# Kernel optimization log

Hardware: AMD Instinct MI355X
Metric: run time of the kernel (lower is better)

The kernel has to match this reference:

```python
import jax, jax.numpy as jnp
import numpy as np

THRESH = 1.0      # membrane_threshold
DECAY = 0.95      # membrane_decay
REFRAC = 2.0      # refractory_period
LR = 0.001        # learning_rate
MAX_RATE = 100.0  # max_spike_rate
DT = 1.0          # time_step (ms)


def _lif(v, r, I):
    """Event-driven LIF update, vectorized over (batch, neuron).
    Neurons are only updated where input current > 0 (as in the original
    gated per-element loop); elsewhere state is frozen.
    """
    active = I > 0
    refrac = r > 0
    v_int = v * DECAY + I
    fired = active & (~refrac) & (v_int >= THRESH)
    v_new = jnp.where(~active, v, jnp.where(refrac | fired, 0.0, v_int))
    r_new = jnp.where(~active, r,
                      jnp.where(refrac, r - 1.0,
                                jnp.where(fired, REFRAC, r)))
    return v_new, r_new, fired.astype(I.dtype)


def setup_inputs() -> dict:
    key = jax.random.key(0)
    k1, k2, k3, k4 = jax.random.split(key, 4)
    B, In, H, Out, T = 128, 1024, 4096, 1024, 100
    x = jax.random.uniform(k1, (B, In), dtype=jnp.float32)
    W1 = jax.random.normal(k2, (H, In), dtype=jnp.float32) / np.float32(np.sqrt(In))
    W2 = jax.random.normal(k3, (Out, H), dtype=jnp.float32) / np.float32(np.sqrt(H))
    noise = jax.random.uniform(k4, (T, B, In), dtype=jnp.float32)
    return {"x": x, "W1": W1, "W2": W2, "noise": noise, "time_steps": T}


def reference(x, W1, W2, noise, time_steps):
    B, In = x.shape
    H = W1.shape[0]
    Out = W2.shape[0]
    # rate coding: Bernoulli spikes per time step  -> (T, B, In)
    probs = jnp.clip(x * MAX_RATE, 0.0, MAX_RATE) * (DT / 1000.0)
    spikes_in = (noise < probs[None]).astype(x.dtype)

    def step(carry, inp):
        v_i, r_i, v_h, r_h, v_o, r_o, W1c, tp, tn, acc = carry
        t, s_in = inp
        # input layer LIF (current = encoded spikes)
        v_i, r_i, in_spk = _lif(v_i, r_i, s_in)
        # hidden layer: current = input spikes @ W1^T
        hid_I = in_spk @ W1c.T                      # (B, H)
        v_h, r_h, hid_spk = _lif(v_h, r_h, hid_I)
        # output layer: current = hidden spikes @ W2^T
        out_I = hid_spk @ W2.T                      # (B, Out)
        v_o, r_o, out_spk = _lif(v_o, r_o, out_I)
        acc = acc + out_spk
        # STDP every 10 steps
        stdp = (t % 10) == 0
        pre_m = in_spk.mean(0)                      # (In,)
        post_m = hid_spk.mean(0)                    # (H,)
        tp_n = 0.9 * tp + pre_m
        tn_n = 0.9 * tn + post_m
        tp = jnp.where(stdp, tp_n, tp)
        tn = jnp.where(stdp, tn_n, tn)
        both = (in_spk.sum() > 0) & (hid_spk.sum() > 0)
        dW = LR * (jnp.outer(tp_n, post_m).T - jnp.outer(pre_m, tn_n).T)  # (H, In)
        W1_new = jnp.clip(W1c + dW, -1.0, 1.0)
        W1c = jnp.where(stdp & both, W1_new, W1c)
        return (v_i, r_i, v_h, r_h, v_o, r_o, W1c, tp, tn, acc), None

    z = lambda *s: jnp.zeros(s, x.dtype)
    carry0 = (z(B, In), z(B, In), z(B, H), z(B, H), z(B, Out), z(B, Out),
              W1, z(In), z(H), z(B, Out))
    xs = (jnp.arange(time_steps), spikes_in)
    carry, _ = jax.lax.scan(step, carry0, xs)
    out_counts = carry[-1]
    return out_counts / time_steps
```

## Files before the change

### kernel.cpp

```cpp
#include <hip/hip_runtime.h>
#include <cstdint>
#include <cstddef>

#define BB   128
#define IN   1024
#define HID  4096
#define OUTN 1024
#define TSTEPS 100
#define KC   384

__global__ __launch_bounds__(256) void ttrans_k(const float* __restrict__ src,
                                                float* __restrict__ dst,
                                                int R, int C) {
  __shared__ float tile[32][33];
  int tx = threadIdx.x & 31;
  int ty = threadIdx.x >> 5;
  int c0 = blockIdx.x * 32, r0 = blockIdx.y * 32;
  #pragma unroll
  for (int j = 0; j < 32; j += 8)
    tile[ty + j][tx] = src[(size_t)(r0 + ty + j) * C + (c0 + tx)];
  __syncthreads();
  #pragma unroll
  for (int j = 0; j < 32; j += 8)
    dst[(size_t)(c0 + ty + j) * R + (r0 + tx)] = tile[tx][ty + j];
}

__device__ __forceinline__ unsigned char lif_f32(float I, float& v, float& r) {
  bool active = I > 0.0f;
  bool refrac = r > 0.0f;
  float vi = __fadd_rn(__fmul_rn(v, 0.95f), I);
  bool fired = active && !refrac && (vi >= 1.0f);
  float vn = !active ? v : ((refrac || fired) ? 0.0f : vi);
  float rn = !active ? r : (refrac ? (r - 1.0f) : (fired ? 2.0f : r));
  v = vn; r = rn;
  return fired ? (unsigned char)1 : (unsigned char)0;
}

__device__ __forceinline__ void hidden_body(
    int bx, int b, int tid,
    const float* __restrict__ noise_t, const float* __restrict__ x,
    const float* __restrict__ rin_in, float* __restrict__ rin_out,
    unsigned char* __restrict__ in_spk,
    const float* __restrict__ W1T,
    float* __restrict__ v_h, float* __restrict__ r_h,
    unsigned char* __restrict__ hid_spk,
    unsigned short* s_idx, int* s_off, int* wsum) {
  size_t ebase = (size_t)b * IN + (size_t)tid * 4;
  const float4 xv = *reinterpret_cast<const float4*>(x + ebase);
  const float4 nv = *reinterpret_cast<const float4*>(noise_t + ebase);
  const float4 rv = *reinterpret_cast<const float4*>(rin_in + ebase);
  float px[4] = {xv.x, xv.y, xv.z, xv.w};
  float pn[4] = {nv.x, nv.y, nv.z, nv.w};
  float pr[4] = {rv.x, rv.y, rv.z, rv.w};
  int f[4]; float rn[4];
  #pragma unroll
  for (int j = 0; j < 4; j++) {
    float p = __fmul_rn(px[j], 100.0f);
    p = fminf(fmaxf(p, 0.0f), 100.0f);
    p = __fmul_rn(p, 0.001f);
    bool s = pn[j] < p;
    bool refrac = pr[j] > 0.0f;
    bool fired = s && !refrac;
    rn[j] = !s ? pr[j] : (refrac ? (pr[j] - 1.0f) : 2.0f);
    f[j] = fired ? 1 : 0;
  }
  if (bx == 0) {
    *reinterpret_cast<float4*>(rin_out + ebase) = make_float4(rn[0], rn[1], rn[2], rn[3]);
    uchar4 sp; sp.x = (unsigned char)f[0]; sp.y = (unsigned char)f[1];
    sp.z = (unsigned char)f[2]; sp.w = (unsigned char)f[3];
    *reinterpret_cast<uchar4*>(in_spk + ebase) = sp;
  }
  int cnt = f[0] + f[1] + f[2] + f[3];

  int lane = tid & 63, wv = tid >> 6;
  int inc = cnt;
  #pragma unroll
  for (int d = 1; d < 64; d <<= 1) {
    int nn = __shfl_up(inc, d, 64);
    if (lane >= d) inc += nn;
  }
  if (lane == 63) wsum[wv] = inc;
  __syncthreads();
  int wbase = 0;
  #pragma unroll
  for (int w = 0; w < 4; w++) if (w < wv) wbase += wsum[w];
  int excl = wbase + inc - cnt;

  int o = excl, kb = tid * 4;
  if (f[0]) s_idx[o++] = (unsigned short)(kb);
  if (f[1]) s_idx[o++] = (unsigned short)(kb + 1);
  if (f[2]) s_idx[o++] = (unsigned short)(kb + 2);
  if (f[3]) s_idx[o++] = (unsigned short)(kb + 3);
  if (tid == 0)   s_off[0] = 0;
  if (tid == 96)  s_off[1] = excl;
  if (tid == 192) s_off[2] = excl;
  if (tid == 255) s_off[3] = excl + cnt;
  __syncthreads();

  int h0 = bx * 1024 + tid * 4;
  const char* Wb = (const char*)W1T;
  unsigned cb = (unsigned)h0 << 2;
  float t0 = 0.0f, t1 = 0.0f, t2 = 0.0f, t3 = 0.0f;
  #pragma unroll
  for (int p = 0; p < 3; p++) {
    int ks = s_off[p], ke = s_off[p + 1];
    float a0 = 0.0f, a1 = 0.0f, a2 = 0.0f, a3 = 0.0f;
    int k = ks;
    for (; k + 4 <= ke; k += 4) {
      unsigned o0 = ((unsigned)s_idx[k]     << 14) + cb;
      unsigned o1 = ((unsigned)s_idx[k + 1] << 14) + cb;
      unsigned o2 = ((unsigned)s_idx[k + 2] << 14) + cb;
      unsigned o3 = ((unsigned)s_idx[k + 3] << 14) + cb;
      float4 w0 = *reinterpret_cast<const float4*>(Wb + o0);
      float4 w1 = *reinterpret_cast<const float4*>(Wb + o1);
      float4 w2 = *reinterpret_cast<const float4*>(Wb + o2);
      float4 w3 = *reinterpret_cast<const float4*>(Wb + o3);
      a0 = __fadd_rn(a0, w0.x); a1 = __fadd_rn(a1, w0.y);
      a2 = __fadd_rn(a2, w0.z); a3 = __fadd_rn(a3, w0.w);
      a0 = __fadd_rn(a0, w1.x); a1 = __fadd_rn(a1, w1.y);
      a2 = __fadd_rn(a2, w1.z); a3 = __fadd_rn(a3, w1.w);
      a0 = __fadd_rn(a0, w2.x); a1 = __fadd_rn(a1, w2.y);
      a2 = __fadd_rn(a2, w2.z); a3 = __fadd_rn(a3, w2.w);
      a0 = __fadd_rn(a0, w3.x); a1 = __fadd_rn(a1, w3.y);
      a2 = __fadd_rn(a2, w3.z); a3 = __fadd_rn(a3, w3.w);
    }
    for (; k < ke; k++) {
      unsigned oo = ((unsigned)s_idx[k] << 14) + cb;
      float4 w = *reinterpret_cast<const float4*>(Wb + oo);
      a0 = __fadd_rn(a0, w.x); a1 = __fadd_rn(a1, w.y);
      a2 = __fadd_rn(a2, w.z); a3 = __fadd_rn(a3, w.w);
    }
    t0 = __fadd_rn(t0, a0); t1 = __fadd_rn(t1, a1);
    t2 = __fadd_rn(t2, a2); t3 = __fadd_rn(t3, a3);
  }
  size_t idx = (size_t)b * HID + h0;
  float4 vv = *reinterpret_cast<float4*>(v_h + idx);
  float4 rr = *reinterpret_cast<float4*>(r_h + idx);
  uchar4 sp;
  sp.x = lif_f32(t0, vv.x, rr.x);
  sp.y = lif_f32(t1, vv.y, rr.y);
  sp.z = lif_f32(t2, vv.z, rr.z);
  sp.w = lif_f32(t3, vv.w, rr.w);
  *reinterpret_cast<float4*>(v_h + idx) = vv;
  *reinterpret_cast<float4*>(r_h + idx) = rr;
  *reinterpret_cast<uchar4*>(hid_spk + idx) = sp;
}

__device__ __forceinline__ void out_body(
    int bx, int b, int tid,
    const unsigned char* __restrict__ hid_spk,
    const float* __restrict__ W2T,
    float* __restrict__ v_o, float* __restrict__ r_o,
    float* __restrict__ out_acc,
    unsigned short* s_idx, int* s_off, int* wsum, float* parts) {
  int lane = tid & 63, kg = tid >> 6;

  uint4 u = *reinterpret_cast<const uint4*>(hid_spk + (size_t)b * HID + tid * 16);
  unsigned ww[4] = {u.x, u.y, u.z, u.w};
  int cnt = 0;
  #pragma unroll
  for (int j = 0; j < 16; j++) cnt += (ww[j >> 2] >> ((j & 3) * 8)) & 0xff;

  int inc = cnt;
  #pragma unroll
  for (int d = 1; d < 64; d <<= 1) {
    int nn = __shfl_up(inc, d, 64);
    if (lane >= d) inc += nn;
  }
  if (lane == 63) wsum[kg] = inc;
  __syncthreads();
  int wbase = 0;
  #pragma unroll
  for (int w = 0; w < 4; w++) if (w < kg) wbase += wsum[w];
  int excl = wbase + inc - cnt;

  int oo = excl, kb = tid * 16;
  #pragma unroll
  for (int j = 0; j < 16; j++) {
    if ((ww[j >> 2] >> ((j & 3) * 8)) & 0xff) s_idx[oo++] = (unsigned short)(kb + j);
  }
  if ((tid % 24) == 0 && tid <= 240) s_off[tid / 24] = excl;
  if (tid == 255) s_off[11] = excl + cnt;
  __syncthreads();

  const int pstart = (kg == 0) ? 0 : (kg == 1) ? 3 : (kg == 2) ? 6 : 9;
  const int pend   = (kg == 0) ? 3 : (kg == 1) ? 6 : (kg == 2) ? 9 : 11;
  int col0 = lane * 4;
  const char* Wb = (const char*)W2T;
  unsigned cb = ((unsigned)(bx * 256 + col0)) << 2;
  for (int p = pstart; p < pend; p++) {
    int ks = s_off[p], ke = s_off[p + 1];
    float a0 = 0.0f, a1 = 0.0f, a2 = 0.0f, a3 = 0.0f;
    int k = ks;
    for (; k + 4 <= ke; k += 4) {
      unsigned o0 = ((unsigned)s_idx[k]     << 12) + cb;
      unsigned o1 = ((unsigned)s_idx[k + 1] << 12) + cb;
      unsigned o2 = ((unsigned)s_idx[k + 2] << 12) + cb;
      unsigned o3 = ((unsigned)s_idx[k + 3] << 12) + cb;
      float4 w0 = *reinterpret_cast<const float4*>(Wb + o0);
      float4 w1 = *reinterpret_cast<const float4*>(Wb + o1);
      float4 w2 = *reinterpret_cast<const float4*>(Wb + o2);
      float4 w3 = *reinterpret_cast<const float4*>(Wb + o3);
      a0 = __fadd_rn(a0, w0.x); a1 = __fadd_rn(a1, w0.y);
      a2 = __fadd_rn(a2, w0.z); a3 = __fadd_rn(a3, w0.w);
      a0 = __fadd_rn(a0, w1.x); a1 = __fadd_rn(a1, w1.y);
      a2 = __fadd_rn(a2, w1.z); a3 = __fadd_rn(a3, w1.w);
      a0 = __fadd_rn(a0, w2.x); a1 = __fadd_rn(a1, w2.y);
      a2 = __fadd_rn(a2, w2.z); a3 = __fadd_rn(a3, w2.w);
      a0 = __fadd_rn(a0, w3.x); a1 = __fadd_rn(a1, w3.y);
      a2 = __fadd_rn(a2, w3.z); a3 = __fadd_rn(a3, w3.w);
    }
    for (; k < ke; k++) {
      unsigned ob = ((unsigned)s_idx[k] << 12) + cb;
      float4 w = *reinterpret_cast<const float4*>(Wb + ob);
      a0 = __fadd_rn(a0, w.x); a1 = __fadd_rn(a1, w.y);
      a2 = __fadd_rn(a2, w.z); a3 = __fadd_rn(a3, w.w);
    }
    *reinterpret_cast<float4*>(parts + p * 256 + col0) = make_float4(a0, a1, a2, a3);
  }
  __syncthreads();

  float total = 0.0f;
  #pragma unroll
  for (int p = 0; p < 11; p++) total = __fadd_rn(total, parts[p * 256 + tid]);
  int o = bx * 256 + tid;
  size_t idx = (size_t)b * OUTN + o;
  float v = v_o[idx], r = r_o[idx];
  unsigned char fired = lif_f32(total, v, r);
  v_o[idx] = v; r_o[idx] = r;
  if (fired) out_acc[idx] = __fadd_rn(out_acc[idx], 1.0f);
}

__global__ __launch_bounds__(256) void hidden_k(
    const float* __restrict__ noise_t, const float* __restrict__ x,
    const float* __restrict__ rin_in, float* __restrict__ rin_out,
    unsigned char* __restrict__ in_spk,
    const float* __restrict__ W1T,
    float* __restrict__ v_h, float* __restrict__ r_h,
    unsigned char* __restrict__ hid_spk) {
  __shared__ unsigned short s_idx[IN];
  __shared__ int s_off[4];
  __shared__ int wsum[4];
  hidden_body(blockIdx.x, blockIdx.y, threadIdx.x, noise_t, x, rin_in, rin_out,
              in_spk, W1T, v_h, r_h, hid_spk, s_idx, s_off, wsum);
}

__global__ __launch_bounds__(256) void out_k(
    const unsigned char* __restrict__ hid_spk, const float* __restrict__ W2T,
    float* __restrict__ v_o, float* __restrict__ r_o, float* __restrict__ out_acc) {
  __shared__ unsigned short s_idx[HID];
  __shared__ int s_off[12];
  __shared__ int wsum[4];
  __shared__ float parts[11 * 256];
  out_body(blockIdx.x, blockIdx.y, threadIdx.x, hid_spk, W2T, v_o, r_o, out_acc,
           s_idx, s_off, wsum, parts);
}

__global__ __launch_bounds__(256) void step_k(
    const float* __restrict__ noise_t, const float* __restrict__ x,
    const float* __restrict__ rin_in, float* __restrict__ rin_out,
    unsigned char* __restrict__ in_spk,
    const float* __restrict__ W1T,
    float* __restrict__ v_h, float* __restrict__ r_h,
    unsigned char* __restrict__ hid_spk_w,
    const unsigned char* __restrict__ hid_spk_r,
    const float* __restrict__ W2T,
    float* __restrict__ v_o, float* __restrict__ r_o, float* __restrict__ out_acc) {
  __shared__ __align__(16) unsigned char smem[19520];
  int b = blockIdx.y;
  if (blockIdx.x < 4) {
    unsigned short* s_idx = (unsigned short*)smem;
    int* s_off = (int*)(smem + 2048);
    int* wsum  = (int*)(smem + 2064);
    hidden_body(blockIdx.x, b, threadIdx.x, noise_t, x, rin_in, rin_out,
                in_spk, W1T, v_h, r_h, hid_spk_w, s_idx, s_off, wsum);
  } else {
    unsigned short* s_idx = (unsigned short*)smem;
    int* s_off = (int*)(smem + 8192);
    int* wsum  = (int*)(smem + 8240);
    float* parts = (float*)(smem + 8256);
    out_body(blockIdx.x - 4, b, threadIdx.x, hid_spk_r, W2T, v_o, r_o, out_acc,
             s_idx, s_off, wsum, parts);
  }
}

#define NWSTAT ((IN + HID) / 4)
__global__ __launch_bounds__(256) void stats1_k(
    const unsigned char* __restrict__ in_spk, const unsigned char* __restrict__ hid_spk,
    unsigned* __restrict__ pcnt) {
  int w = blockIdx.x * 256 + threadIdx.x;
  int r0 = blockIdx.y * 16;
  unsigned s = 0;
  if (w < IN / 4) {
    const unsigned* p = (const unsigned*)in_spk;
    #pragma unroll
    for (int b = 0; b < 16; b++) s += p[(size_t)(r0 + b) * (IN / 4) + w];
  } else {
    const unsigned* p = (const unsigned*)hid_spk;
    int w2 = w - IN / 4;
    #pragma unroll
    for (int b = 0; b < 16; b++) s += p[(size_t)(r0 + b) * (HID / 4) + w2];
  }
  atomicAdd(pcnt + w, s);
}

__global__ __launch_bounds__(256) void stats2_k(
    const unsigned* __restrict__ pcnt,
    float* __restrict__ pre_m, float* __restrict__ post_m,
    float* __restrict__ tp, float* __restrict__ tn, int* __restrict__ flags) {
  int c = blockIdx.x * 256 + threadIdx.x;
  int cnt = (int)((pcnt[c >> 2] >> ((c & 3) * 8)) & 0xff);
  int lane = threadIdx.x & 63;
  if (c < IN) {
    float pm = __fdiv_rn((float)cnt, 128.0f);
    pre_m[c] = pm;
    tp[c] = __fadd_rn(__fmul_rn(0.9f, tp[c]), pm);
    unsigned long long any = __ballot(cnt > 0);
    if (any && lane == 0) atomicOr(flags + 0, 1);
  } else {
    int h = c - IN;
    float pm = __fdiv_rn((float)cnt, 128.0f);
    post_m[h] = pm;
    tn[h] = __fadd_rn(__fmul_rn(0.9f, tn[h]), pm);
    unsigned long long any = __ballot(cnt > 0);
    if (any && lane == 0) atomicOr(flags + 1, 1);
  }
}

__global__ __launch_bounds__(256) void apply_k(
    float* __restrict__ W1T,
    const float* __restrict__ tp, const float* __restrict__ tn,
    const float* __restrict__ pre_m, const float* __restrict__ post_m,
    const int* __restrict__ flags) {
  if (!(flags[0] && flags[1])) return;
  size_t idx = (size_t)blockIdx.x * 256 + threadIdx.x;
  int i = (int)(idx >> 12);
  int h = (int)(idx & 4095);
  float a  = __fmul_rn(tp[i], post_m[h]);
  float b2 = __fmul_rn(pre_m[i], tn[h]);
  float d  = __fmul_rn(0.001f, __fsub_rn(a, b2));
  float w  = __fadd_rn(W1T[idx], d);
  w = fminf(fmaxf(w, -1.0f), 1.0f);
  W1T[idx] = w;
}

__global__ __launch_bounds__(256) void scale_k(const float* __restrict__ acc,
                                               float* __restrict__ out) {
  int j = blockIdx.x * 256 + threadIdx.x;
  out[j] = __fdiv_rn(acc[j], 100.0f);
}

extern "C" void kernel_launch(void* const* d_in, const int* in_sizes, int n_in,
                              void* d_out, int out_size, void* d_ws, size_t ws_size,
                              hipStream_t stream) {
  (void)in_sizes; (void)n_in; (void)out_size; (void)ws_size;
  const float* x     = (const float*)d_in[0];
  const float* W1    = (const float*)d_in[1];
  const float* W2    = (const float*)d_in[2];
  const float* noise = (const float*)d_in[3];

  char* ws = (char*)d_ws;
  size_t off = 0;
  auto alloc = [&](size_t bytes) -> char* {
    char* p = ws + off;
    off += (bytes + 255) & ~(size_t)255;
    return p;
  };
  float* W1T   = (float*)alloc((size_t)IN * HID * 4);
  float* W2T   = (float*)alloc((size_t)HID * OUTN * 4);
  float* v_h   = (float*)alloc((size_t)BB * HID * 4);
  float* r_h   = (float*)alloc((size_t)BB * HID * 4);
  float* v_o   = (float*)alloc((size_t)BB * OUTN * 4);
  float* r_o   = (float*)alloc((size_t)BB * OUTN * 4);
  float* rinA  = (float*)alloc((size_t)BB * IN * 4);
  float* rinB  = (float*)alloc((size_t)BB * IN * 4);
  float* acc   = (float*)alloc((size_t)BB * OUTN * 4);
  float* tp    = (float*)alloc((size_t)IN * 4);
  float* tn    = (float*)alloc((size_t)HID * 4);
  float* pre_m = (float*)alloc((size_t)IN * 4);
  float* post_m= (float*)alloc((size_t)HID * 4);
  unsigned char* in_spk   = (unsigned char*)alloc((size_t)BB * IN);
  unsigned char* hid_spkA = (unsigned char*)alloc((size_t)BB * HID);
  unsigned char* hid_spkB = (unsigned char*)alloc((size_t)BB * HID);
  unsigned* pcnt = (unsigned*)alloc((size_t)10 * NWSTAT * 4);
  int* flags   = (int*)alloc(2 * 10 * sizeof(int));

  hipMemsetAsync(v_h, 0, (size_t)BB * HID * 4, stream);
  hipMemsetAsync(r_h, 0, (size_t)BB * HID * 4, stream);
  hipMemsetAsync(v_o, 0, (size_t)BB * OUTN * 4, stream);
  hipMemsetAsync(r_o, 0, (size_t)BB * OUTN * 4, stream);
  hipMemsetAsync(rinA, 0, (size_t)BB * IN * 4, stream);
  hipMemsetAsync(acc, 0, (size_t)BB * OUTN * 4, stream);
  hipMemsetAsync(tp,  0, (size_t)IN * 4, stream);
  hipMemsetAsync(tn,  0, (size_t)HID * 4, stream);
  hipMemsetAsync(pcnt, 0, (size_t)10 * NWSTAT * 4, stream);
  hipMemsetAsync(flags, 0, 2 * 10 * sizeof(int), stream);

  ttrans_k<<<dim3(IN / 32, HID / 32), 256, 0, stream>>>(W1, W1T, HID, IN);
  ttrans_k<<<dim3(HID / 32, OUTN / 32), 256, 0, stream>>>(W2, W2T, OUTN, HID);

  float* rin_in = rinA;
  float* rin_out = rinB;

  hidden_k<<<dim3(HID / 1024, BB), 256, 0, stream>>>(noise, x, rin_in, rin_out, in_spk,
                                                     W1T, v_h, r_h, hid_spkA);
  {
    unsigned* pc = pcnt;  int* fl = flags;
    stats1_k<<<dim3(NWSTAT / 256, 8), 256, 0, stream>>>(in_spk, hid_spkA, pc);
    stats2_k<<<(IN + HID) / 256, 256, 0, stream>>>(pc, pre_m, post_m, tp, tn, fl);
    apply_k<<<(IN * HID) / 256, 256, 0, stream>>>(W1T, tp, tn, pre_m, post_m, fl);
  }
  { float* tmpp = rin_in; rin_in = rin_out; rin_out = tmpp; }

  for (int t = 1; t < TSTEPS; t++) {
    const float* nz = noise + (size_t)t * BB * IN;
    unsigned char* hs_w = (t & 1) ? hid_spkB : hid_spkA;
    unsigned char* hs_r = (t & 1) ? hid_spkA : hid_spkB;
    step_k<<<dim3(8, BB), 256, 0, stream>>>(nz, x, rin_in, rin_out, in_spk,
                                            W1T, v_h, r_h, hs_w, hs_r,
                                            W2T, v_o, r_o, acc);
    if (t % 10 == 0) {
      unsigned* pc = pcnt + (size_t)NWSTAT * (t / 10);
      int* fl = flags + 2 * (t / 10);
      stats1_k<<<dim3(NWSTAT / 256, 8), 256, 0, stream>>>(in_spk, hs_w, pc);
      stats2_k<<<(IN + HID) / 256, 256, 0, stream>>>(pc, pre_m, post_m, tp, tn, fl);
      apply_k<<<(IN * HID) / 256, 256, 0, stream>>>(W1T, tp, tn, pre_m, post_m, fl);
    }
    float* tmpp = rin_in; rin_in = rin_out; rin_out = tmpp;
  }

  unsigned char* hs_last = ((TSTEPS - 1) & 1) ? hid_spkB : hid_spkA;
  out_k<<<dim3(OUTN / 256, BB), 256, 0, stream>>>(hs_last, W2T, v_o, r_o, acc);

  scale_k<<<(BB * OUTN) / 256, 256, 0, stream>>>(acc, (float*)d_out);
}
```

Before: 1.501 ms.

## Unroll gathers by eight and fold STDP stats kernel into apply kernel

Replaces the 4-wide sparse weight-gather loops in the hidden and output stages with a shared 8-wide unrolled macro, aiming to keep more independent loads in flight. Removes the stats2 kernel: apply2 now recomputes spike means and trace updates per element from the packed counts, with double-buffered tp/tn arrays so the trace reads and writes do not race. The any-spike flags are now set in stats1, and its batch split is doubled. This saves one launch per STDP step, at the cost of extra redundant arithmetic and register pressure in apply2 and the gather loops.

```diff
diff --git a/kernel.cpp b/kernel.cpp
--- a/kernel.cpp
+++ b/kernel.cpp
@@ -35,6 +35,70 @@
   v = vn; r = rn;
   return fired ? (unsigned char)1 : (unsigned char)0;
 }
+
+#define GATHER8(SH)                                                              \
+  {                                                                              \
+    int k = ks;                                                                  \
+    for (; k + 8 <= ke; k += 8) {                                                \
+      unsigned o0 = ((unsigned)s_idx[k]     << SH) + cb;                         \
+      unsigned o1 = ((unsigned)s_idx[k + 1] << SH) + cb;                         \
+      unsigned o2 = ((unsigned)s_idx[k + 2] << SH) + cb;                         \
+      unsigned o3 = ((unsigned)s_idx[k + 3] << SH) + cb;                         \
+      unsigned o4 = ((unsigned)s_idx[k + 4] << SH) + cb;                         \
+      unsigned o5 = ((unsigned)s_idx[k + 5] << SH) + cb;                         \
+      unsigned o6 = ((unsigned)s_idx[k + 6] << SH) + cb;                         \
+      unsigned o7 = ((unsigned)s_idx[k + 7] << SH) + cb;                         \
+      float4 w0 = *reinterpret_cast<const float4*>(Wb + o0);                     \
+      float4 w1 = *reinterpret_cast<const float4*>(Wb + o1);                     \
+      float4 w2 = *reinterpret_cast<const float4*>(Wb + o2);                     \
+      float4 w3 = *reinterpret_cast<const float4*>(Wb + o3);                     \
+      float4 w4 = *reinterpret_cast<const float4*>(Wb + o4);                     \
+      float4 w5 = *reinterpret_cast<const float4*>(Wb + o5);                     \
+      float4 w6 = *reinterpret_cast<const float4*>(Wb + o6);                     \
+      float4 w7 = *reinterpret_cast<const float4*>(Wb + o7);                     \
+      a0 = __fadd_rn(a0, w0.x); a1 = __fadd_rn(a1, w0.y);                        \
+      a2 = __fadd_rn(a2, w0.z); a3 = __fadd_rn(a3, w0.w);                        \
+      a0 = __fadd_rn(a0, w1.x); a1 = __fadd_rn(a1, w1.y);                        \
+      a2 = __fadd_rn(a2, w1.z); a3 = __fadd_rn(a3, w1.w);                        \
+      a0 = __fadd_rn(a0, w2.x); a1 = __fadd_rn(a1, w2.y);                        \
+      a2 = __fadd_rn(a2, w2.z); a3 = __fadd_rn(a3, w2.w);                        \
+      a0 = __fadd_rn(a0, w3.x); a1 = __fadd_rn(a1, w3.y);                        \
+      a2 = __fadd_rn(a2, w3.z); a3 = __fadd_rn(a3, w3.w);                        \
+      a0 = __fadd_rn(a0, w4.x); a1 = __fadd_rn(a1, w4.y);                        \
+      a2 = __fadd_rn(a2, w4.z); a3 = __fadd_rn(a3, w4.w);                        \
+      a0 = __fadd_rn(a0, w5.x); a1 = __fadd_rn(a1, w5.y);                        \
+      a2 = __fadd_rn(a2, w5.z); a3 = __fadd_rn(a3, w5.w);                        \
+      a0 = __fadd_rn(a0, w6.x); a1 = __fadd_rn(a1, w6.y);                        \
+      a2 = __fadd_rn(a2, w6.z); a3 = __fadd_rn(a3, w6.w);                        \
+      a0 = __fadd_rn(a0, w7.x); a1 = __fadd_rn(a1, w7.y);                        \
+      a2 = __fadd_rn(a2, w7.z); a3 = __fadd_rn(a3, w7.w);                        \
+    }                                                                            \
+    if (k + 4 <= ke) {                                                           \
+      unsigned o0 = ((unsigned)s_idx[k]     << SH) + cb;                         \
+      unsigned o1 = ((unsigned)s_idx[k + 1] << SH) + cb;                         \
+      unsigned o2 = ((unsigned)s_idx[k + 2] << SH) + cb;                         \
+      unsigned o3 = ((unsigned)s_idx[k + 3] << SH) + cb;                         \
+      float4 w0 = *reinterpret_cast<const float4*>(Wb + o0);                     \
+      float4 w1 = *reinterpret_cast<const float4*>(Wb + o1);                     \
+      float4 w2 = *reinterpret_cast<const float4*>(Wb + o2);                     \
+      float4 w3 = *reinterpret_cast<const float4*>(Wb + o3);                     \
+      a0 = __fadd_rn(a0, w0.x); a1 = __fadd_rn(a1, w0.y);                        \
+      a2 = __fadd_rn(a2, w0.z); a3 = __fadd_rn(a3, w0.w);                        \
+      a0 = __fadd_rn(a0, w1.x); a1 = __fadd_rn(a1, w1.y);                        \
+      a2 = __fadd_rn(a2, w1.z); a3 = __fadd_rn(a3, w1.w);                        \
+      a0 = __fadd_rn(a0, w2.x); a1 = __fadd_rn(a1, w2.y);                        \
+      a2 = __fadd_rn(a2, w2.z); a3 = __fadd_rn(a3, w2.w);                        \
+      a0 = __fadd_rn(a0, w3.x); a1 = __fadd_rn(a1, w3.y);                        \
+      a2 = __fadd_rn(a2, w3.z); a3 = __fadd_rn(a3, w3.w);                        \
+      k += 4;                                                                    \
+    }                                                                            \
+    for (; k < ke; k++) {                                                        \
+      unsigned oo = ((unsigned)s_idx[k] << SH) + cb;                             \
+      float4 w = *reinterpret_cast<const float4*>(Wb + oo);                      \
+      a0 = __fadd_rn(a0, w.x); a1 = __fadd_rn(a1, w.y);                          \
+      a2 = __fadd_rn(a2, w.z); a3 = __fadd_rn(a3, w.w);                          \
+    }                                                                            \
+  }
 
 __device__ __forceinline__ void hidden_body(
     int bx, int b, int tid,
@@ -105,31 +169,7 @@
   for (int p = 0; p < 3; p++) {
     int ks = s_off[p], ke = s_off[p + 1];
     float a0 = 0.0f, a1 = 0.0f, a2 = 0.0f, a3 = 0.0f;
-    int k = ks;
-    for (; k + 4 <= ke; k += 4) {
-      unsigned o0 = ((unsigned)s_idx[k]     << 14) + cb;
-      unsigned o1 = ((unsigned)s_idx[k + 1] << 14) + cb;
-      unsigned o2 = ((unsigned)s_idx[k + 2] << 14) + cb;
-      unsigned o3 = ((unsigned)s_idx[k + 3] << 14) + cb;
-      float4 w0 = *reinterpret_cast<const float4*>(Wb + o0);
-      float4 w1 = *reinterpret_cast<const float4*>(Wb + o1);
-      float4 w2 = *reinterpret_cast<const float4*>(Wb + o2);
-      float4 w3 = *reinterpret_cast<const float4*>(Wb + o3);
-      a0 = __fadd_rn(a0, w0.x); a1 = __fadd_rn(a1, w0.y);
-      a2 = __fadd_rn(a2, w0.z); a3 = __fadd_rn(a3, w0.w);
-      a0 = __fadd_rn(a0, w1.x); a1 = __fadd_rn(a1, w1.y);
-      a2 = __fadd_rn(a2, w1.z); a3 = __fadd_rn(a3, w1.w);
-      a0 = __fadd_rn(a0, w2.x); a1 = __fadd_rn(a1, w2.y);
-      a2 = __fadd_rn(a2, w2.z); a3 = __fadd_rn(a3, w2.w);
-      a0 = __fadd_rn(a0, w3.x); a1 = __fadd_rn(a1, w3.y);
-      a2 = __fadd_rn(a2, w3.z); a3 = __fadd_rn(a3, w3.w);
-    }
-    for (; k < ke; k++) {
-      unsigned oo = ((unsigned)s_idx[k] << 14) + cb;
-      float4 w = *reinterpret_cast<const float4*>(Wb + oo);
-      a0 = __fadd_rn(a0, w.x); a1 = __fadd_rn(a1, w.y);
-      a2 = __fadd_rn(a2, w.z); a3 = __fadd_rn(a3, w.w);
-    }
+    GATHER8(14)
     t0 = __fadd_rn(t0, a0); t1 = __fadd_rn(t1, a1);
     t2 = __fadd_rn(t2, a2); t3 = __fadd_rn(t3, a3);
   }
@@ -191,31 +231,7 @@
   for (int p = pstart; p < pend; p++) {
     int ks = s_off[p], ke = s_off[p + 1];
     float a0 = 0.0f, a1 = 0.0f, a2 = 0.0f, a3 = 0.0f;
-    int k = ks;
-    for (; k + 4 <= ke; k += 4) {
-      unsigned o0 = ((unsigned)s_idx[k]     << 12) + cb;
-      unsigned o1 = ((unsigned)s_idx[k + 1] << 12) + cb;
-      unsigned o2 = ((unsigned)s_idx[k + 2] << 12) + cb;
-      unsigned o3 = ((unsigned)s_idx[k + 3] << 12) + cb;
-      float4 w0 = *reinterpret_cast<const float4*>(Wb + o0);
-      float4 w1 = *reinterpret_cast<const float4*>(Wb + o1);
-      float4 w2 = *reinterpret_cast<const float4*>(Wb + o2);
-      float4 w3 = *reinterpret_cast<const float4*>(Wb + o3);
-      a0 = __fadd_rn(a0, w0.x); a1 = __fadd_rn(a1, w0.y);
-      a2 = __fadd_rn(a2, w0.z); a3 = __fadd_rn(a3, w0.w);
-      a0 = __fadd_rn(a0, w1.x); a1 = __fadd_rn(a1, w1.y);
-      a2 = __fadd_rn(a2, w1.z); a3 = __fadd_rn(a3, w1.w);
-      a0 = __fadd_rn(a0, w2.x); a1 = __fadd_rn(a1, w2.y);
-      a2 = __fadd_rn(a2, w2.z); a3 = __fadd_rn(a3, w2.w);
-      a0 = __fadd_rn(a0, w3.x); a1 = __fadd_rn(a1, w3.y);
-      a2 = __fadd_rn(a2, w3.z); a3 = __fadd_rn(a3, w3.w);
-    }
-    for (; k < ke; k++) {
-      unsigned ob = ((unsigned)s_idx[k] << 12) + cb;
-      float4 w = *reinterpret_cast<const float4*>(Wb + ob);
-      a0 = __fadd_rn(a0, w.x); a1 = __fadd_rn(a1, w.y);
-      a2 = __fadd_rn(a2, w.z); a3 = __fadd_rn(a3, w.w);
-    }
+    GATHER8(12)
     *reinterpret_cast<float4*>(parts + p * 256 + col0) = make_float4(a0, a1, a2, a3);
   }
   __syncthreads();
@@ -287,57 +303,50 @@
 #define NWSTAT ((IN + HID) / 4)
 __global__ __launch_bounds__(256) void stats1_k(
     const unsigned char* __restrict__ in_spk, const unsigned char* __restrict__ hid_spk,
-    unsigned* __restrict__ pcnt) {
+    unsigned* __restrict__ pcnt, int* __restrict__ flags) {
   int w = blockIdx.x * 256 + threadIdx.x;
-  int r0 = blockIdx.y * 16;
+  int r0 = blockIdx.y * 8;
+  int lane = threadIdx.x & 63;
   unsigned s = 0;
   if (w < IN / 4) {
     const unsigned* p = (const unsigned*)in_spk;
     #pragma unroll
-    for (int b = 0; b < 16; b++) s += p[(size_t)(r0 + b) * (IN / 4) + w];
+    for (int b = 0; b < 8; b++) s += p[(size_t)(r0 + b) * (IN / 4) + w];
+    atomicAdd(pcnt + w, s);
+    unsigned long long any = __ballot(s > 0);
+    if (any && lane == 0) atomicOr(flags + 0, 1);
   } else {
     const unsigned* p = (const unsigned*)hid_spk;
     int w2 = w - IN / 4;
     #pragma unroll
-    for (int b = 0; b < 16; b++) s += p[(size_t)(r0 + b) * (HID / 4) + w2];
-  }
-  atomicAdd(pcnt + w, s);
-}
-
-__global__ __launch_bounds__(256) void stats2_k(
+    for (int b = 0; b < 8; b++) s += p[(size_t)(r0 + b) * (HID / 4) + w2];
+    atomicAdd(pcnt + w, s);
+    unsigned long long any = __ballot(s > 0);
+    if (any && lane == 0) atomicOr(flags + 1, 1);
+  }
+}
+
+__global__ __launch_bounds__(256) void apply2_k(
+    float* __restrict__ W1T,
     const unsigned* __restrict__ pcnt,
-    float* __restrict__ pre_m, float* __restrict__ post_m,
-    float* __restrict__ tp, float* __restrict__ tn, int* __restrict__ flags) {
-  int c = blockIdx.x * 256 + threadIdx.x;
-  int cnt = (int)((pcnt[c >> 2] >> ((c & 3) * 8)) & 0xff);
-  int lane = threadIdx.x & 63;
-  if (c < IN) {
-    float pm = __fdiv_rn((float)cnt, 128.0f);
-    pre_m[c] = pm;
-    tp[c] = __fadd_rn(__fmul_rn(0.9f, tp[c]), pm);
-    unsigned long long any = __ballot(cnt > 0);
-    if (any && lane == 0) atomicOr(flags + 0, 1);
-  } else {
-    int h = c - IN;
-    float pm = __fdiv_rn((float)cnt, 128.0f);
-    post_m[h] = pm;
-    tn[h] = __fadd_rn(__fmul_rn(0.9f, tn[h]), pm);
-    unsigned long long any = __ballot(cnt > 0);
-    if (any && lane == 0) atomicOr(flags + 1, 1);
-  }
-}
-
-__global__ __launch_bounds__(256) void apply_k(
-    float* __restrict__ W1T,
-    const float* __restrict__ tp, const float* __restrict__ tn,
-    const float* __restrict__ pre_m, const float* __restrict__ post_m,
+    const float* __restrict__ tp_in, float* __restrict__ tp_out,
+    const float* __restrict__ tn_in, float* __restrict__ tn_out,
     const int* __restrict__ flags) {
-  if (!(flags[0] && flags[1])) return;
   size_t idx = (size_t)blockIdx.x * 256 + threadIdx.x;
   int i = (int)(idx >> 12);
   int h = (int)(idx & 4095);
-  float a  = __fmul_rn(tp[i], post_m[h]);
-  float b2 = __fmul_rn(pre_m[i], tn[h]);
+  int cnt_i = (int)((pcnt[i >> 2] >> ((i & 3) * 8)) & 0xff);
+  int ch = IN + h;
+  int cnt_h = (int)((pcnt[ch >> 2] >> ((ch & 3) * 8)) & 0xff);
+  float pm_i = __fmul_rn((float)cnt_i, 0.0078125f);
+  float pm_h = __fmul_rn((float)cnt_h, 0.0078125f);
+  float tpn = __fadd_rn(__fmul_rn(0.9f, tp_in[i]), pm_i);
+  float tnn = __fadd_rn(__fmul_rn(0.9f, tn_in[h]), pm_h);
+  if (h == 0) tp_out[i] = tpn;
+  if (i == 0) tn_out[h] = tnn;
+  if (!(flags[0] && flags[1])) return;
+  float a  = __fmul_rn(tpn, pm_h);
+  float b2 = __fmul_rn(pm_i, tnn);
   float d  = __fmul_rn(0.001f, __fsub_rn(a, b2));
   float w  = __fadd_rn(W1T[idx], d);
   w = fminf(fmaxf(w, -1.0f), 1.0f);
@@ -375,10 +384,10 @@
   float* rinA  = (float*)alloc((size_t)BB * IN * 4);
   float* rinB  = (float*)alloc((size_t)BB * IN * 4);
   float* acc   = (float*)alloc((size_t)BB * OUTN * 4);
-  float* tp    = (float*)alloc((size_t)IN * 4);
-  float* tn    = (float*)alloc((size_t)HID * 4);
-  float* pre_m = (float*)alloc((size_t)IN * 4);
-  float* post_m= (float*)alloc((size_t)HID * 4);
+  float* tpA   = (float*)alloc((size_t)IN * 4);
+  float* tpB   = (float*)alloc((size_t)IN * 4);
+  float* tnA   = (float*)alloc((size_t)HID * 4);
+  float* tnB   = (float*)alloc((size_t)HID * 4);
   unsigned char* in_spk   = (unsigned char*)alloc((size_t)BB * IN);
   unsigned char* hid_spkA = (unsigned char*)alloc((size_t)BB * HID);
   unsigned char* hid_spkB = (unsigned char*)alloc((size_t)BB * HID);
@@ -391,8 +400,8 @@
   hipMemsetAsync(r_o, 0, (size_t)BB * OUTN * 4, stream);
   hipMemsetAsync(rinA, 0, (size_t)BB * IN * 4, stream);
   hipMemsetAsync(acc, 0, (size_t)BB * OUTN * 4, stream);
-  hipMemsetAsync(tp,  0, (size_t)IN * 4, stream);
-  hipMemsetAsync(tn,  0, (size_t)HID * 4, stream);
+  hipMemsetAsync(tpA, 0, (size_t)IN * 4, stream);
+  hipMemsetAsync(tnA, 0, (size_t)HID * 4, stream);
   hipMemsetAsync(pcnt, 0, (size_t)10 * NWSTAT * 4, stream);
   hipMemsetAsync(flags, 0, 2 * 10 * sizeof(int), stream);
 
@@ -401,14 +410,18 @@
 
   float* rin_in = rinA;
   float* rin_out = rinB;
+  float* tp_in = tpA; float* tp_out = tpB;
+  float* tn_in = tnA; float* tn_out = tnB;
 
   hidden_k<<<dim3(HID / 1024, BB), 256, 0, stream>>>(noise, x, rin_in, rin_out, in_spk,
                                                      W1T, v_h, r_h, hid_spkA);
   {
     unsigned* pc = pcnt;  int* fl = flags;
-    stats1_k<<<dim3(NWSTAT / 256, 8), 256, 0, stream>>>(in_spk, hid_spkA, pc);
-    stats2_k<<<(IN + HID) / 256, 256, 0, stream>>>(pc, pre_m, post_m, tp, tn, fl);
-    apply_k<<<(IN * HID) / 256, 256, 0, stream>>>(W1T, tp, tn, pre_m, post_m, fl);
+    stats1_k<<<dim3(NWSTAT / 256, 16), 256, 0, stream>>>(in_spk, hid_spkA, pc, fl);
+    apply2_k<<<(IN * HID) / 256, 256, 0, stream>>>(W1T, pc, tp_in, tp_out,
+                                                   tn_in, tn_out, fl);
+    float* t1 = tp_in; tp_in = tp_out; tp_out = t1;
+    float* t2 = tn_in; tn_in = tn_out; tn_out = t2;
   }
   { float* tmpp = rin_in; rin_in = rin_out; rin_out = tmpp; }
 
@@ -422,9 +435,11 @@
     if (t % 10 == 0) {
       unsigned* pc = pcnt + (size_t)NWSTAT * (t / 10);
       int* fl = flags + 2 * (t / 10);
-      stats1_k<<<dim3(NWSTAT / 256, 8), 256, 0, stream>>>(in_spk, hs_w, pc);
-      stats2_k<<<(IN + HID) / 256, 256, 0, stream>>>(pc, pre_m, post_m, tp, tn, fl);
-      apply_k<<<(IN * HID) / 256, 256, 0, stream>>>(W1T, tp, tn, pre_m, post_m, fl);
+      stats1_k<<<dim3(NWSTAT / 256, 16), 256, 0, stream>>>(in_spk, hs_w, pc, fl);
+      apply2_k<<<(IN * HID) / 256, 256, 0, stream>>>(W1T, pc, tp_in, tp_out,
+                                                     tn_in, tn_out, fl);
+      float* t1 = tp_in; tp_in = tp_out; tp_out = t1;
+      float* t2 = tn_in; tn_in = tn_out; tn_out = t2;
     }
     float* tmpp = rin_in; rin_in = rin_out; rin_out = tmpp;
   }
```

Result: no change. 1.487 ms (-0.9%).
